# Kernel optimization log

Hardware: AMD Instinct MI355X
Metric: run time of the kernel (lower is better)

The kernel has to match this reference:

```python
import jax, jax.numpy as jnp
import numpy as np

B, T, V, D, H, L = 4, 2048, 99, 512, 8, 6
DH = D // H
OFFSET = 28  # size_puzzle_tokens = 1 + 26 + 1
GELU_C = 0.7978845608028654  # sqrt(2/pi)
EPS = 1e-5


def layernorm(x, w):
    m = jnp.mean(x, axis=-1, keepdims=True)
    v = jnp.mean(jnp.square(x - m), axis=-1, keepdims=True)
    return (x - m) / jnp.sqrt(v + EPS) * w


def new_gelu(x):
    return 0.5 * x * (1.0 + jnp.tanh(GELU_C * (x + 0.044715 * x ** 3)))


def setup_inputs() -> dict:
    key = jax.random.key(0)
    ks = jax.random.split(key, 12)
    s = 0.02
    return {
        'idx': jax.random.randint(ks[0], (B, T), 0, V),
        'targets': jax.random.randint(ks[1], (B, T), 0, V),
        'wte': jax.random.normal(ks[2], (V, D), jnp.float32) * s,   # tied with lm_head
        'wpe': jax.random.normal(ks[3], (T, D), jnp.float32) * s,
        'ln1_w': jnp.ones((L, D), jnp.float32),
        'attn_w': jax.random.normal(ks[4], (L, 3 * D, D), jnp.float32) * s,
        'proj_w': jax.random.normal(ks[5], (L, D, D), jnp.float32) * (s / np.sqrt(2 * L)),
        'ln2_w': jnp.ones((L, D), jnp.float32),
        'fc_w': jax.random.normal(ks[6], (L, 4 * D, D), jnp.float32) * s,
        'fc_proj_w': jax.random.normal(ks[7], (L, D, 4 * D), jnp.float32) * (s / np.sqrt(2 * L)),
        'lnf_w': jnp.ones((D,), jnp.float32),
    }


def _forward(idx, targets, wte, wpe, ln1_w, attn_w, proj_w, ln2_w, fc_w, fc_proj_w, lnf_w):
    t = idx.shape[1]
    x = wte[idx] + wpe[:t][None]  # [B,T,D]
    # mask: tril(ones(T+28, T)) narrowed from row 28 -> query i attends keys j <= i+28
    q_ids = jnp.arange(t)
    mask = (q_ids[None, :] <= q_ids[:, None] + OFFSET)  # [T,T]
    scale = 1.0 / np.sqrt(DH)

    def block(x, p):
        w1, wa, wp, w2, wf, wfp = p
        h = layernorm(x, w1)
        qkv = jnp.einsum('btc,oc->bto', h, wa)  # [B,T,3D]
        q, k, v = jnp.split(qkv, 3, axis=-1)
        q = q.reshape(B, t, H, DH)
        k = k.reshape(B, t, H, DH)
        v = v.reshape(B, t, H, DH)
        att = jnp.einsum('bqhd,bkhd->bhqk', q, k) * scale
        att = jnp.where(mask[None, None], att, -jnp.inf)
        att = jax.nn.softmax(att, axis=-1)
        y = jnp.einsum('bhqk,bkhd->bqhd', att, v).reshape(B, t, D)
        y = jnp.einsum('btc,oc->bto', y, wp)
        x = x + y
        h2 = layernorm(x, w2)
        m = new_gelu(jnp.einsum('btc,fc->btf', h2, wf))
        x = x + jnp.einsum('btf,cf->btc', m, wfp)
        return x, None

    x, _ = jax.lax.scan(block, x, (ln1_w, attn_w, proj_w, ln2_w, fc_w, fc_proj_w))
    x = layernorm(x, lnf_w)
    logits = jnp.einsum('btd,vd->btv', x, wte)

    # weighted cross entropy, ignore_index=-1
    ce_w = jnp.zeros((V,), jnp.float32).at[78:96].set(1.0).at[96].set(0.1)
    y = targets.reshape(-1)
    valid = (y != -1)
    yc = jnp.where(valid, y, 0)
    logp = jax.nn.log_softmax(logits.reshape(-1, V), axis=-1)
    nll = -jnp.take_along_axis(logp, yc[:, None], axis=1)[:, 0]
    wi = ce_w[yc] * valid.astype(jnp.float32)
    loss = jnp.sum(wi * nll) / jnp.sum(wi)
    return logits, loss


def reference(idx, targets, wte, wpe, ln1_w, attn_w, proj_w, ln2_w, fc_w, fc_proj_w, lnf_w):
    return _forward(idx, targets, wte, wpe, ln1_w, attn_w, proj_w, ln2_w, fc_w, fc_proj_w, lnf_w)
```

## Files before the change

kernel.cpp:

```cpp
#include <hip/hip_runtime.h>
#include <hip/hip_bf16.h>
#include <math.h>

#define BB 4
#define TT 2048
#define VV 99
#define DD 512
#define HH 8
#define LL 6
#define DHH 64
#define OFFS 28
#define ROWS (BB*TT)

typedef __hip_bfloat16 bf16;
typedef __attribute__((ext_vector_type(8))) short bf16x8;
typedef __attribute__((ext_vector_type(4))) short s16x4;
typedef __attribute__((ext_vector_type(4))) float f32x4;

__device__ __forceinline__ float b2f(bf16 x){ return __bfloat162float(x); }

__device__ __forceinline__ void async_copy16(const void* g, void* l){
    __builtin_amdgcn_global_load_lds(
        (const __attribute__((address_space(1))) unsigned int*)g,
        (__attribute__((address_space(3))) unsigned int*)l, 16, 0, 0);
}

__device__ __forceinline__ unsigned lds_off(const void* p){
    return (unsigned)(size_t)(const __attribute__((address_space(3))) char*)p;
}

#define TRD(dst, a, lit) asm volatile("ds_read_b64_tr_b16 %0, %1 offset:" lit \
                                      : "=v"(dst) : "v"(a) : "memory")
#define CAT8(lo, hi) ((bf16x8)__builtin_shufflevector((lo), (hi), 0,1,2,3,4,5,6,7))

__device__ __forceinline__ unsigned pk2(float a, float b){
    return ((unsigned)(unsigned short)__bfloat16_as_short(__float2bfloat16(a)))
         | ((unsigned)(unsigned short)__bfloat16_as_short(__float2bfloat16(b)) << 16);
}

__device__ __forceinline__ float wget(const void* w, int mode, size_t i){
    return mode ? b2f(((const bf16*)w)[i]) : ((const float*)w)[i];
}

__global__ void init_kernel(const unsigned int* __restrict__ ln1_bits, float* __restrict__ acc,
                            int* __restrict__ flag){
    acc[0] = 0.f; acc[1] = 0.f;
    flag[0] = (ln1_bits[0] == 0x3F800000u) ? 0 : 1;
}

__global__ __launch_bounds__(256) void wconv_kernel(const void* __restrict__ src,
                                                    bf16* __restrict__ dst, int n,
                                                    const int* __restrict__ flag){
    int mode = flag[0];
    size_t i0 = ((size_t)blockIdx.x*256 + threadIdx.x)*8;
    if (i0 >= (size_t)n) return;
    if (mode == 0){
        const float4* sp = (const float4*)((const float*)src + i0);
        float4 a = sp[0], b = sp[1];
        float f[8] = {a.x,a.y,a.z,a.w, b.x,b.y,b.z,b.w};
        union { short s[8]; uint4 u; } cv;
        #pragma unroll
        for (int k=0;k<8;++k) cv.s[k] = __bfloat16_as_short(__float2bfloat16(f[k]));
        *(uint4*)(dst + i0) = cv.u;
    } else {
        *(uint4*)(dst + i0) = *(const uint4*)((const bf16*)src + i0);
    }
}

__global__ void embed_kernel(const int* __restrict__ idx, const void* __restrict__ wte,
                             const void* __restrict__ wpe, float* __restrict__ x,
                             const int* __restrict__ flag){
    int mode = flag[0];
    int row = blockIdx.x;
    int t = row % TT;
    int tok = idx[row];
    int i = threadIdx.x;
    #pragma unroll
    for (int j = 0; j < 2; ++j){
        int d = i + j*256;
        x[(size_t)row*DD + d] = wget(wte, mode, (size_t)tok*DD + d)
                              + wget(wpe, mode, (size_t)t*DD + d);
    }
}

__global__ void ln_kernel(const float* __restrict__ x, const void* __restrict__ w,
                          size_t woff, bf16* __restrict__ out, const int* __restrict__ flag){
    int mode = flag[0];
    int row = blockIdx.x;
    int lane = threadIdx.x;
    const float* xr = x + (size_t)row*DD;
    float v[8];
    float s = 0.f;
    #pragma unroll
    for (int j=0;j<8;++j){ v[j] = xr[lane + j*64]; s += v[j]; }
    #pragma unroll
    for (int o=32;o;o>>=1) s += __shfl_xor(s,o);
    float mean = s * (1.0f/DD);
    float vs = 0.f;
    #pragma unroll
    for (int j=0;j<8;++j){ float d = v[j]-mean; vs += d*d; }
    #pragma unroll
    for (int o=32;o;o>>=1) vs += __shfl_xor(vs,o);
    float rstd = rsqrtf(vs*(1.0f/DD) + 1e-5f);
    #pragma unroll
    for (int j=0;j<8;++j){
        int d = lane + j*64;
        out[(size_t)row*DD + d] = __float2bfloat16((v[j]-mean)*rstd*wget(w,mode,woff+d));
    }
}

template<int EPI>
__global__ __launch_bounds__(256) void gemm_mfma(const bf16* __restrict__ A,
        const bf16* __restrict__ W, float* __restrict__ C, bf16* __restrict__ Cb,
        int M, int N, int K){
    __shared__ short As[128*32];
    __shared__ short Ws[128*32];
    int tid = threadIdx.x;
    int m0 = blockIdx.y * 128;
    int n0 = blockIdx.x * 128;
    int lane = tid & 63, wave = tid >> 6;
    int wm = (wave & 1) * 64, wn = (wave >> 1) * 64;
    int quad = lane >> 4, l16 = lane & 15;

    f32x4 acc[4][4] = {};

    int srow = wave*16 + (lane >> 2);
    int scol = (lane & 3) * 8;
    const bf16* ga = A + (size_t)(m0 + srow)*K + scol;
    const bf16* gw = W + (size_t)(n0 + srow)*K + scol;
    short* laA0 = &As[(wave*16)*32];
    short* laA1 = &As[(64 + wave*16)*32];
    short* laW0 = &Ws[(wave*16)*32];
    short* laW1 = &Ws[(64 + wave*16)*32];

    for (int k0 = 0; k0 < K; k0 += 32){
        __syncthreads();
        async_copy16(ga + k0,                 laA0);
        async_copy16(ga + (size_t)64*K + k0,  laA1);
        async_copy16(gw + k0,                 laW0);
        async_copy16(gw + (size_t)64*K + k0,  laW1);
        __syncthreads();

        bf16x8 af[4], bfr[4];
        #pragma unroll
        for (int mi=0;mi<4;++mi)
            af[mi] = *(const bf16x8*)&As[(wm + mi*16 + l16)*32 + quad*8];
        #pragma unroll
        for (int ni=0;ni<4;++ni)
            bfr[ni] = *(const bf16x8*)&Ws[(wn + ni*16 + l16)*32 + quad*8];
        #pragma unroll
        for (int mi=0;mi<4;++mi)
            #pragma unroll
            for (int ni=0;ni<4;++ni)
                acc[mi][ni] = __builtin_amdgcn_mfma_f32_16x16x32_bf16(af[mi], bfr[ni], acc[mi][ni], 0, 0, 0);
    }

    #pragma unroll
    for (int mi=0;mi<4;++mi){
        #pragma unroll
        for (int ni=0;ni<4;++ni){
            int mg = m0 + wm + mi*16 + quad*4;
            int ng = n0 + wn + ni*16 + l16;
            #pragma unroll
            for (int reg=0;reg<4;++reg){
                float val = acc[mi][ni][reg];
                size_t off = (size_t)(mg+reg)*N + ng;
                if (EPI==0){
                    Cb[off] = __float2bfloat16(val);
                } else {
                    float xx = val;
                    float u = 0.7978845608028654f*(xx + 0.044715f*xx*xx*xx);
                    Cb[off] = __float2bfloat16(0.5f*xx*(1.0f+tanhf(u)));
                }
            }
        }
    }
}

__global__ __launch_bounds__(256) void gemm_mfma64(const bf16* __restrict__ A,
        const bf16* __restrict__ W, float* __restrict__ C, int M, int N, int K){
    __shared__ short As[64*32];
    __shared__ short Ws[128*32];
    int tid = threadIdx.x;
    int m0 = blockIdx.y * 64;
    int n0 = blockIdx.x * 128;
    int lane = tid & 63, wave = tid >> 6;
    int wm = (wave & 1) * 32, wn = (wave >> 1) * 64;
    int quad = lane >> 4, l16 = lane & 15;

    f32x4 acc[2][4] = {};

    int srow = wave*16 + (lane >> 2);
    int scol = (lane & 3) * 8;
    const bf16* ga = A + (size_t)(m0 + srow)*K + scol;
    const bf16* gw = W + (size_t)(n0 + srow)*K + scol;
    short* laA0 = &As[(wave*16)*32];
    short* laW0 = &Ws[(wave*16)*32];
    short* laW1 = &Ws[(64 + wave*16)*32];

    for (int k0 = 0; k0 < K; k0 += 32){
        __syncthreads();
        async_copy16(ga + k0,                 laA0);
        async_copy16(gw + k0,                 laW0);
        async_copy16(gw + (size_t)64*K + k0,  laW1);
        __syncthreads();

        bf16x8 af[2], bfr[4];
        #pragma unroll
        for (int mi=0;mi<2;++mi)
            af[mi] = *(const bf16x8*)&As[(wm + mi*16 + l16)*32 + quad*8];
        #pragma unroll
        for (int ni=0;ni<4;++ni)
            bfr[ni] = *(const bf16x8*)&Ws[(wn + ni*16 + l16)*32 + quad*8];
        #pragma unroll
        for (int mi=0;mi<2;++mi)
            #pragma unroll
            for (int ni=0;ni<4;++ni)
                acc[mi][ni] = __builtin_amdgcn_mfma_f32_16x16x32_bf16(af[mi], bfr[ni], acc[mi][ni], 0, 0, 0);
    }

    #pragma unroll
    for (int mi=0;mi<2;++mi){
        #pragma unroll
        for (int ni=0;ni<4;++ni){
            int mg = m0 + wm + mi*16 + quad*4;
            int ng = n0 + wn + ni*16 + l16;
            #pragma unroll
            for (int reg=0;reg<4;++reg){
                C[(size_t)(mg+reg)*N + ng] += acc[mi][ni][reg];
            }
        }
    }
}

__global__ __launch_bounds__(256) void gemm_nt3(const bf16* __restrict__ A,
        const void* __restrict__ W, size_t woff, float* __restrict__ C,
        int M, int N, int K, const int* __restrict__ flag){
    int mode = flag[0];
    __shared__ float As[16][64];
    __shared__ float Wt[16][64];
    int m0 = blockIdx.y * 64;
    int n0 = blockIdx.x * 64;
    int t = threadIdx.x;
    int tx = t & 15, ty = t >> 4;
    float acc[4][4] = {};
    int am = t >> 2;
    int ak = (t & 3) * 4;

    for (int k0 = 0; k0 < K; k0 += 16){
        {
            const __hip_bfloat162* ap = (const __hip_bfloat162*)(A + (size_t)(m0+am)*K + k0 + ak);
            __hip_bfloat162 p0 = ap[0], p1 = ap[1];
            float2 f0 = __bfloat1622float2(p0), f1 = __bfloat1622float2(p1);
            As[ak+0][am]=f0.x; As[ak+1][am]=f0.y; As[ak+2][am]=f1.x; As[ak+3][am]=f1.y;
        }
        int wn = n0 + am;
        if (wn < N){
            size_t off = woff + (size_t)wn*K + k0 + ak;
            if (mode == 0){
                float4 wv = *(const float4*)((const float*)W + off);
                Wt[ak+0][am]=wv.x; Wt[ak+1][am]=wv.y; Wt[ak+2][am]=wv.z; Wt[ak+3][am]=wv.w;
            } else {
                const __hip_bfloat162* wp = (const __hip_bfloat162*)((const bf16*)W + off);
                __hip_bfloat162 p0 = wp[0], p1 = wp[1];
                float2 f0 = __bfloat1622float2(p0), f1 = __bfloat1622float2(p1);
                Wt[ak+0][am]=f0.x; Wt[ak+1][am]=f0.y; Wt[ak+2][am]=f1.x; Wt[ak+3][am]=f1.y;
            }
        } else {
            Wt[ak+0][am]=0.f; Wt[ak+1][am]=0.f; Wt[ak+2][am]=0.f; Wt[ak+3][am]=0.f;
        }
        __syncthreads();
        #pragma unroll
        for (int kk=0;kk<16;++kk){
            float a[4], b[4];
            #pragma unroll
            for (int i=0;i<4;++i) a[i]=As[kk][ty*4+i];
            #pragma unroll
            for (int j=0;j<4;++j) b[j]=Wt[kk][tx*4+j];
            #pragma unroll
            for (int i=0;i<4;++i)
                #pragma unroll
                for (int j=0;j<4;++j)
                    acc[i][j] += a[i]*b[j];
        }
        __syncthreads();
    }

    #pragma unroll
    for (int i=0;i<4;++i){
        int m = m0 + ty*4 + i;
        #pragma unroll
        for (int j=0;j<4;++j){
            int n = n0 + tx*4 + j;
            if (n >= N) continue;
            C[(size_t)m*N+n] = acc[i][j];
        }
    }
}

__global__ __launch_bounds__(256) void attn_mfma11(const bf16* __restrict__ qkv,
                                                   bf16* __restrict__ y){
    __shared__ __align__(16) short Ks[4][4096];
    __shared__ __align__(16) short Vs[4][4096];
    __shared__ __align__(16) short P2[4][1024];

    int tid = threadIdx.x;
    int lane = tid & 63, wave = tid >> 6;
    int quad = lane >> 4, l16 = lane & 15;

    int bi = blockIdx.x;
    int qt = 31 - (bi >> 5);
    int bh = bi & 31;
    int h = bh & 7;
    int b = bh >> 3;
    int q0 = qt * 64;
    size_t base = (size_t)b * TT * 1536;

    const bf16* qrow = qkv + base + (size_t)(q0 + wave*16 + l16)*1536 + h*64;
    bf16x8 aq0 = *(const bf16x8*)(qrow + quad*8);
    bf16x8 aq1 = *(const bf16x8*)(qrow + 32 + quad*8);

    int kj  = wave*16 + (lane>>3);
    int kgo = ((lane&7) ^ ((lane>>3)&7)) << 3;
    int vj  = ((lane>>3)&3)*8 + ((lane>>5)&1)*4 + ((lane>>1)&3);
    int vdo = wave*16 + ((lane&1)<<3);
    const bf16* ks0 = qkv + base + DD   + h*64 + (size_t)kj*1536 + kgo;
    const bf16* vs0 = qkv + base + 2*DD + h*64 + (size_t)vj*1536 + vdo;
    short* kd = &Ks[0][0] + wave*1024;
    short* vd = &Vs[0][0] + wave*1024;

#define STAGE(bb, j0s) { \
    const bf16* kk_ = ks0 + (size_t)(j0s)*1536; \
    const bf16* vv_ = vs0 + (size_t)(j0s)*1536; \
    short* kdd_ = kd + (bb)*4096; \
    short* vdd_ = vd + (bb)*4096; \
    async_copy16(kk_,                    kdd_); \
    async_copy16(kk_ + (size_t)8*1536,   kdd_ + 512); \
    async_copy16(vv_,                    vdd_); \
    async_copy16(vv_ + (size_t)32*1536,  vdd_ + 512); }

    f32x4 O[4] = {};
    float mr1 = -1e30f;
    float lr1 = 0.f;

    int jbmax = qt + 1; if (jbmax > 31) jbmax = 31;
    int NT = jbmax + 1;

    STAGE(0, 0);
    if (NT > 1) STAGE(1, 64);
    __syncthreads();

    unsigned l8 = (unsigned)(lane << 3);
    unsigned vbase = lds_off(&Vs[0][0]) + l8;
    char* pw = (char*)&P2[wave][0];
    int swz = (l16 & 7) << 4;
    int qg_row = q0 + wave*16 + l16;
    int sb = (quad<<4) | (quad<<2);

#define ATTN_BODY(tt) { \
    int t_ = (tt); \
    int j0 = t_ * 64; \
    const short* kb = &Ks[0][0] + (t_&3)*4096; \
    f32x4 s4[4]; \
    _Pragma("unroll") \
    for (int ni=0; ni<4; ++ni){ \
        int R = ni*16 + l16; \
        int ro = R*64; \
        int sw = R & 7; \
        bf16x8 bk0 = *(const bf16x8*)&kb[ro + ((quad       ^ sw)<<3)]; \
        bf16x8 bk1 = *(const bf16x8*)&kb[ro + (((quad + 4) ^ sw)<<3)]; \
        f32x4 z = {}; \
        z = __builtin_amdgcn_mfma_f32_16x16x32_bf16(bk0, aq0, z, 0, 0, 0); \
        z = __builtin_amdgcn_mfma_f32_16x16x32_bf16(bk1, aq1, z, 0, 0, 0); \
        s4[ni] = z; \
    } \
    float sc[4][4]; \
    bool bd = (j0 + 63 > q0 + OFFS); \
    _Pragma("unroll") \
    for (int ni=0; ni<4; ++ni){ \
        _Pragma("unroll") \
        for (int reg=0; reg<4; ++reg){ \
            float v = s4[ni][reg] * 0.125f; \
            if (bd){ \
                int jg = j0 + ni*16 + quad*4 + reg; \
                if (jg > qg_row + OFFS) v = -1e30f; \
            } \
            sc[ni][reg] = v; \
        } \
    } \
    float mn[4]; \
    _Pragma("unroll") \
    for (int ni=0; ni<4; ++ni) \
        mn[ni] = fmaxf(fmaxf(sc[ni][0], sc[ni][1]), fmaxf(sc[ni][2], sc[ni][3])); \
    float m16 = fmaxf(fmaxf(mn[0], mn[1]), fmaxf(mn[2], mn[3])); \
    m16 = fmaxf(m16, __shfl_xor(m16, 16)); \
    m16 = fmaxf(m16, __shfl_xor(m16, 32)); \
    float nm; \
    float alpha1 = 1.0f; \
    if (__all(m16 <= mr1 + 8.0f)){ \
        nm = mr1;             \
    } else { \
        nm = fmaxf(mr1, m16); \
        alpha1 = __expf(mr1 - nm); \
        mr1 = nm; \
        float al0 = __shfl(alpha1, sb); \
        float al1 = __shfl(alpha1, sb+1); \
        float al2 = __shfl(alpha1, sb+2); \
        float al3 = __shfl(alpha1, sb+3); \
        _Pragma("unroll") \
        for (int dt=0; dt<4; ++dt){ \
            O[dt][0] *= al0; O[dt][1] *= al1; O[dt][2] *= al2; O[dt][3] *= al3; \
        } \
    } \
    float rsn[4]; \
    _Pragma("unroll") \
    for (int ni=0; ni<4; ++ni){ \
        _Pragma("unroll") \
        for (int reg=0; reg<4; ++reg) \
            sc[ni][reg] = __expf(sc[ni][reg] - nm); \
        rsn[ni] = (sc[ni][0] + sc[ni][1]) + (sc[ni][2] + sc[ni][3]); \
    } \
    float rs1 = (rsn[0] + rsn[1]) + (rsn[2] + rsn[3]); \
    rs1 += __shfl_xor(rs1, 16); \
    rs1 += __shfl_xor(rs1, 32); \
    lr1 = lr1*alpha1 + rs1; \
    __builtin_amdgcn_sched_barrier(0); \
    unsigned va = vbase + (unsigned)((t_&3)*8192); \
    s16x4 t000,t001,t010,t011, t100,t101,t110,t111, \
          t200,t201,t210,t211, t300,t301,t310,t311; \
    TRD(t000, va, "0");    TRD(t001, va, "512");  TRD(t010, va, "1024"); TRD(t011, va, "1536"); \
    TRD(t100, va, "2048"); TRD(t101, va, "2560"); TRD(t110, va, "3072"); TRD(t111, va, "3584"); \
    TRD(t200, va, "4096"); TRD(t201, va, "4608"); TRD(t210, va, "5120"); TRD(t211, va, "5632"); \
    TRD(t300, va, "6144"); TRD(t301, va, "6656"); TRD(t310, va, "7168"); TRD(t311, va, "7680"); \
    _Pragma("unroll") \
    for (int ni=0; ni<4; ++ni){ \
        unsigned lo = pk2(sc[ni][0], sc[ni][1]); \
        unsigned hi = pk2(sc[ni][2], sc[ni][3]); \
        *(uint2*)(pw + (((l16<<7) + (ni<<5) + (quad<<3)) ^ swz)) = make_uint2(lo, hi); \
    } \
    bf16x8 ap0 = *(const bf16x8*)(pw + (((l16<<7)      + (quad<<4)) ^ swz)); \
    bf16x8 ap1 = *(const bf16x8*)(pw + (((l16<<7) + 64 + (quad<<4)) ^ swz)); \
    asm volatile("s_waitcnt lgkmcnt(0)" ::: "memory"); \
    __builtin_amdgcn_sched_barrier(0); \
    O[0] = __builtin_amdgcn_mfma_f32_16x16x32_bf16(ap0, CAT8(t000,t001), O[0], 0, 0, 0); \
    O[1] = __builtin_amdgcn_mfma_f32_16x16x32_bf16(ap0, CAT8(t100,t101), O[1], 0, 0, 0); \
    O[2] = __builtin_amdgcn_mfma_f32_16x16x32_bf16(ap0, CAT8(t200,t201), O[2], 0, 0, 0); \
    O[3] = __builtin_amdgcn_mfma_f32_16x16x32_bf16(ap0, CAT8(t300,t301), O[3], 0, 0, 0); \
    O[0] = __builtin_amdgcn_mfma_f32_16x16x32_bf16(ap1, CAT8(t010,t011), O[0], 0, 0, 0); \
    O[1] = __builtin_amdgcn_mfma_f32_16x16x32_bf16(ap1, CAT8(t110,t111), O[1], 0, 0, 0); \
    O[2] = __builtin_amdgcn_mfma_f32_16x16x32_bf16(ap1, CAT8(t210,t211), O[2], 0, 0, 0); \
    O[3] = __builtin_amdgcn_mfma_f32_16x16x32_bf16(ap1, CAT8(t310,t311), O[3], 0, 0, 0); }

    for (int tp = 0; tp < NT; tp += 2){
        if (tp+2 < NT) STAGE((tp+2)&3, (tp+2)*64);
        if (tp+3 < NT) STAGE((tp+3)&3, (tp+3)*64);
        ATTN_BODY(tp);
        if (tp+1 < NT) ATTN_BODY(tp+1);
        __syncthreads();
    }
#undef ATTN_BODY
#undef STAGE

    float invl = 1.0f / lr1;
    float in0 = __shfl(invl, sb);
    float in1 = __shfl(invl, sb+1);
    float in2 = __shfl(invl, sb+2);
    float in3 = __shfl(invl, sb+3);
    float inv[4] = {in0, in1, in2, in3};
    #pragma unroll
    for (int dt=0; dt<4; ++dt){
        #pragma unroll
        for (int reg=0; reg<4; ++reg){
            int qg = q0 + wave*16 + quad*4 + reg;
            y[((size_t)b*TT + qg)*DD + h*64 + dt*16 + l16] =
                __float2bfloat16(O[dt][reg] * inv[reg]);
        }
    }
}

__global__ void loss_kernel(const float* __restrict__ logits, const int* __restrict__ targets,
                            float* __restrict__ acc){
    int row = blockIdx.x;
    int lane = threadIdx.x;
    int yt = targets[row];
    const float* lp = logits + (size_t)row*VV;
    float e0 = (lane < VV)    ? lp[lane]    : -1e30f;
    float e1 = (lane+64 < VV) ? lp[lane+64] : -1e30f;
    float mx = fmaxf(e0,e1);
    #pragma unroll
    for (int o=32;o;o>>=1) mx = fmaxf(mx, __shfl_xor(mx,o));
    float se = 0.f;
    if (lane < VV)    se += __expf(e0-mx);
    if (lane+64 < VV) se += __expf(e1-mx);
    #pragma unroll
    for (int o=32;o;o>>=1) se += __shfl_xor(se,o);
    if (lane == 0 && yt >= 0){
        float wi = (yt>=78 && yt<96) ? 1.0f : (yt==96 ? 0.1f : 0.0f);
        if (wi > 0.f){
            float ly = lp[yt];
            float nll = -(ly - mx - logf(se));
            atomicAdd(&acc[0], wi*nll);
            atomicAdd(&acc[1], wi);
        }
    }
}

__global__ void fin_loss(const float* __restrict__ acc, float* __restrict__ out){
    out[0] = acc[0]/acc[1];
}

extern "C" void kernel_launch(void* const* d_in, const int* in_sizes, int n_in,
                              void* d_out, int out_size, void* d_ws, size_t ws_size,
                              hipStream_t stream){
    const int*  idx     = (const int*) d_in[0];
    const int*  targets = (const int*) d_in[1];
    const void* wte     = d_in[2];
    const void* wpe     = d_in[3];
    const void* ln1_w   = d_in[4];
    const void* attn_w  = d_in[5];
    const void* proj_w  = d_in[6];
    const void* ln2_w   = d_in[7];
    const void* fc_w    = d_in[8];
    const void* fcp_w   = d_in[9];
    const void* lnf_w   = d_in[10];
    float* out = (float*)d_out;

    float* ws   = (float*)d_ws;
    float* ACC  = ws;
    int*   FLAG = (int*)(ws + 4);
    bf16*  Hb   = (bf16*)(ws + 16);
    float* X    = ws + 2097168;
    bf16*  BIG  = (bf16*)(ws + 6291472);
    bf16*  WB   = (bf16*)(ws + 14680080);

    const int ATT_S = 3*DD*DD;
    const int PRJ_S = DD*DD;
    const int FC_S  = 4*DD*DD;
    bf16* WB_att = WB;
    bf16* WB_prj = WB + (size_t)6*ATT_S;
    bf16* WB_fc  = WB_prj + (size_t)6*PRJ_S;
    bf16* WB_fcp = WB_fc  + (size_t)6*FC_S;

    init_kernel<<<1,1,0,stream>>>((const unsigned int*)ln1_w, ACC, FLAG);
    wconv_kernel<<<(6*ATT_S)/2048,256,0,stream>>>(attn_w, WB_att, 6*ATT_S, FLAG);
    wconv_kernel<<<(6*PRJ_S)/2048,256,0,stream>>>(proj_w, WB_prj, 6*PRJ_S, FLAG);
    wconv_kernel<<<(6*FC_S)/2048,256,0,stream>>>(fc_w,  WB_fc,  6*FC_S, FLAG);
    wconv_kernel<<<(6*FC_S)/2048,256,0,stream>>>(fcp_w, WB_fcp, 6*FC_S, FLAG);
    embed_kernel<<<ROWS,256,0,stream>>>(idx, wte, wpe, X, FLAG);
    for (int l=0; l<LL; ++l){
        ln_kernel<<<ROWS,64,0,stream>>>(X, ln1_w, (size_t)l*DD, Hb, FLAG);
        gemm_mfma<0><<<dim3(3*DD/128, ROWS/128),256,0,stream>>>(Hb, WB_att + (size_t)l*ATT_S,
                                                                nullptr, BIG, ROWS, 3*DD, DD);
        attn_mfma11<<<dim3(BB*HH*32),256,0,stream>>>(BIG, Hb);
        gemm_mfma64<<<dim3(DD/128, ROWS/64),256,0,stream>>>(Hb, WB_prj + (size_t)l*PRJ_S,
                                                            X, ROWS, DD, DD);
        ln_kernel<<<ROWS,64,0,stream>>>(X, ln2_w, (size_t)l*DD, Hb, FLAG);
        gemm_mfma<2><<<dim3(4*DD/128, ROWS/128),256,0,stream>>>(Hb, WB_fc + (size_t)l*FC_S,
                                                                nullptr, BIG, ROWS, 4*DD, DD);
        gemm_mfma64<<<dim3(DD/128, ROWS/64),256,0,stream>>>(BIG, WB_fcp + (size_t)l*FC_S,
                                                            X, ROWS, DD, 4*DD);
    }
    ln_kernel<<<ROWS,64,0,stream>>>(X, lnf_w, 0, Hb, FLAG);
    gemm_nt3<<<dim3((VV+63)/64, ROWS/64),256,0,stream>>>(Hb, wte, 0, out, ROWS, VV, DD, FLAG);
    loss_kernel<<<ROWS,64,0,stream>>>(out, targets, ACC);
    fin_loss<<<1,1,0,stream>>>(ACC, out + (size_t)ROWS*VV);
}
```

Baseline: 1.503 ms.

## Double-buffer LDS in MFMA GEMMs and move logits GEMM onto MFMA

Both MFMA GEMM kernels now use two LDS buffers, so the async global-to-LDS copy for the next K-slice is issued before the current slice's MFMAs, and only one barrier runs per iteration instead of two. The scalar fp32 logits GEMM is replaced by an MFMA kernel that reads a bf16 copy of wte, zero-padded to 128 rows by a new conversion kernel. This targets exposed load latency and the slow scalar logits path, at the cost of twice the LDS per block (possibly lowering occupancy), an extra workspace region and bf16 rounding of the tied embedding weights.

```diff
diff --git a/kernel.cpp b/kernel.cpp
--- a/kernel.cpp
+++ b/kernel.cpp
@@ -67,6 +67,22 @@
     }
 }
 
+__global__ __launch_bounds__(256) void wconv_pad(const void* __restrict__ src,
+                                                 bf16* __restrict__ dst, int n, int npad,
+                                                 const int* __restrict__ flag){
+    int mode = flag[0];
+    size_t i0 = ((size_t)blockIdx.x*256 + threadIdx.x)*8;
+    if (i0 >= (size_t)npad) return;
+    union { short s[8]; uint4 u; } cv;
+    #pragma unroll
+    for (int k=0;k<8;++k){
+        size_t i = i0 + k;
+        float f = (i < (size_t)n) ? wget(src, mode, i) : 0.f;
+        cv.s[k] = __bfloat16_as_short(__float2bfloat16(f));
+    }
+    *(uint4*)(dst + i0) = cv.u;
+}
+
 __global__ void embed_kernel(const int* __restrict__ idx, const void* __restrict__ wte,
                              const void* __restrict__ wpe, float* __restrict__ x,
                              const int* __restrict__ flag){
@@ -113,8 +129,8 @@
 __global__ __launch_bounds__(256) void gemm_mfma(const bf16* __restrict__ A,
         const bf16* __restrict__ W, float* __restrict__ C, bf16* __restrict__ Cb,
         int M, int N, int K){
-    __shared__ short As[128*32];
-    __shared__ short Ws[128*32];
+    __shared__ short As[2][128*32];
+    __shared__ short Ws[2][128*32];
     int tid = threadIdx.x;
     int m0 = blockIdx.y * 128;
     int n0 = blockIdx.x * 128;
@@ -128,32 +144,36 @@
     int scol = (lane & 3) * 8;
     const bf16* ga = A + (size_t)(m0 + srow)*K + scol;
     const bf16* gw = W + (size_t)(n0 + srow)*K + scol;
-    short* laA0 = &As[(wave*16)*32];
-    short* laA1 = &As[(64 + wave*16)*32];
-    short* laW0 = &Ws[(wave*16)*32];
-    short* laW1 = &Ws[(64 + wave*16)*32];
+
+#define GSTAGE(bb, kk) { \
+    async_copy16(ga + (kk),                 &As[bb][(wave*16)*32]); \
+    async_copy16(ga + (size_t)64*K + (kk),  &As[bb][(64 + wave*16)*32]); \
+    async_copy16(gw + (kk),                 &Ws[bb][(wave*16)*32]); \
+    async_copy16(gw + (size_t)64*K + (kk),  &Ws[bb][(64 + wave*16)*32]); }
+
+    GSTAGE(0, 0);
+    __syncthreads();
+    int cur = 0;
 
     for (int k0 = 0; k0 < K; k0 += 32){
-        __syncthreads();
-        async_copy16(ga + k0,                 laA0);
-        async_copy16(ga + (size_t)64*K + k0,  laA1);
-        async_copy16(gw + k0,                 laW0);
-        async_copy16(gw + (size_t)64*K + k0,  laW1);
-        __syncthreads();
+        if (k0 + 32 < K) GSTAGE(cur^1, k0 + 32);
 
         bf16x8 af[4], bfr[4];
         #pragma unroll
         for (int mi=0;mi<4;++mi)
-            af[mi] = *(const bf16x8*)&As[(wm + mi*16 + l16)*32 + quad*8];
+            af[mi] = *(const bf16x8*)&As[cur][(wm + mi*16 + l16)*32 + quad*8];
         #pragma unroll
         for (int ni=0;ni<4;++ni)
-            bfr[ni] = *(const bf16x8*)&Ws[(wn + ni*16 + l16)*32 + quad*8];
+            bfr[ni] = *(const bf16x8*)&Ws[cur][(wn + ni*16 + l16)*32 + quad*8];
         #pragma unroll
         for (int mi=0;mi<4;++mi)
             #pragma unroll
             for (int ni=0;ni<4;++ni)
                 acc[mi][ni] = __builtin_amdgcn_mfma_f32_16x16x32_bf16(af[mi], bfr[ni], acc[mi][ni], 0, 0, 0);
-    }
+
+        if (k0 + 32 < K){ __syncthreads(); cur ^= 1; }
+    }
+#undef GSTAGE
 
     #pragma unroll
     for (int mi=0;mi<4;++mi){
@@ -179,8 +199,8 @@
 
 __global__ __launch_bounds__(256) void gemm_mfma64(const bf16* __restrict__ A,
         const bf16* __restrict__ W, float* __restrict__ C, int M, int N, int K){
-    __shared__ short As[64*32];
-    __shared__ short Ws[128*32];
+    __shared__ short As[2][64*32];
+    __shared__ short Ws[2][128*32];
     int tid = threadIdx.x;
     int m0 = blockIdx.y * 64;
     int n0 = blockIdx.x * 128;
@@ -194,30 +214,35 @@
     int scol = (lane & 3) * 8;
     const bf16* ga = A + (size_t)(m0 + srow)*K + scol;
     const bf16* gw = W + (size_t)(n0 + srow)*K + scol;
-    short* laA0 = &As[(wave*16)*32];
-    short* laW0 = &Ws[(wave*16)*32];
-    short* laW1 = &Ws[(64 + wave*16)*32];
+
+#define GSTAGE64(bb, kk) { \
+    async_copy16(ga + (kk),                 &As[bb][(wave*16)*32]); \
+    async_copy16(gw + (kk),                 &Ws[bb][(wave*16)*32]); \
+    async_copy16(gw + (size_t)64*K + (kk),  &Ws[bb][(64 + wave*16)*32]); }
+
+    GSTAGE64(0, 0);
+    __syncthreads();
+    int cur = 0;
 
     for (int k0 = 0; k0 < K; k0 += 32){
-        __syncthreads();
-        async_copy16(ga + k0,                 laA0);
-        async_copy16(gw + k0,                 laW0);
-        async_copy16(gw + (size_t)64*K + k0,  laW1);
-        __syncthreads();
+        if (k0 + 32 < K) GSTAGE64(cur^1, k0 + 32);
 
         bf16x8 af[2], bfr[4];
         #pragma unroll
         for (int mi=0;mi<2;++mi)
-            af[mi] = *(const bf16x8*)&As[(wm + mi*16 + l16)*32 + quad*8];
+            af[mi] = *(const bf16x8*)&As[cur][(wm + mi*16 + l16)*32 + quad*8];
         #pragma unroll
         for (int ni=0;ni<4;++ni)
-            bfr[ni] = *(const bf16x8*)&Ws[(wn + ni*16 + l16)*32 + quad*8];
+            bfr[ni] = *(const bf16x8*)&Ws[cur][(wn + ni*16 + l16)*32 + quad*8];
         #pragma unroll
         for (int mi=0;mi<2;++mi)
             #pragma unroll
             for (int ni=0;ni<4;++ni)
                 acc[mi][ni] = __builtin_amdgcn_mfma_f32_16x16x32_bf16(af[mi], bfr[ni], acc[mi][ni], 0, 0, 0);
-    }
+
+        if (k0 + 32 < K){ __syncthreads(); cur ^= 1; }
+    }
+#undef GSTAGE64
 
     #pragma unroll
     for (int mi=0;mi<2;++mi){
@@ -233,67 +258,64 @@
     }
 }
 
-__global__ __launch_bounds__(256) void gemm_nt3(const bf16* __restrict__ A,
-        const void* __restrict__ W, size_t woff, float* __restrict__ C,
-        int M, int N, int K, const int* __restrict__ flag){
-    int mode = flag[0];
-    __shared__ float As[16][64];
-    __shared__ float Wt[16][64];
-    int m0 = blockIdx.y * 64;
-    int n0 = blockIdx.x * 64;
-    int t = threadIdx.x;
-    int tx = t & 15, ty = t >> 4;
-    float acc[4][4] = {};
-    int am = t >> 2;
-    int ak = (t & 3) * 4;
-
-    for (int k0 = 0; k0 < K; k0 += 16){
-        {
-            const __hip_bfloat162* ap = (const __hip_bfloat162*)(A + (size_t)(m0+am)*K + k0 + ak);
-            __hip_bfloat162 p0 = ap[0], p1 = ap[1];
-            float2 f0 = __bfloat1622float2(p0), f1 = __bfloat1622float2(p1);
-            As[ak+0][am]=f0.x; As[ak+1][am]=f0.y; As[ak+2][am]=f1.x; As[ak+3][am]=f1.y;
-        }
-        int wn = n0 + am;
-        if (wn < N){
-            size_t off = woff + (size_t)wn*K + k0 + ak;
-            if (mode == 0){
-                float4 wv = *(const float4*)((const float*)W + off);
-                Wt[ak+0][am]=wv.x; Wt[ak+1][am]=wv.y; Wt[ak+2][am]=wv.z; Wt[ak+3][am]=wv.w;
-            } else {
-                const __hip_bfloat162* wp = (const __hip_bfloat162*)((const bf16*)W + off);
-                __hip_bfloat162 p0 = wp[0], p1 = wp[1];
-                float2 f0 = __bfloat1622float2(p0), f1 = __bfloat1622float2(p1);
-                Wt[ak+0][am]=f0.x; Wt[ak+1][am]=f0.y; Wt[ak+2][am]=f1.x; Wt[ak+3][am]=f1.y;
-            }
-        } else {
-            Wt[ak+0][am]=0.f; Wt[ak+1][am]=0.f; Wt[ak+2][am]=0.f; Wt[ak+3][am]=0.f;
-        }
-        __syncthreads();
-        #pragma unroll
-        for (int kk=0;kk<16;++kk){
-            float a[4], b[4];
+__global__ __launch_bounds__(256) void gemm_logits(const bf16* __restrict__ A,
+        const bf16* __restrict__ W, float* __restrict__ C){
+    const int K = DD;
+    __shared__ short As[2][128*32];
+    __shared__ short Ws[2][128*32];
+    int tid = threadIdx.x;
+    int m0 = blockIdx.y * 128;
+    int lane = tid & 63, wave = tid >> 6;
+    int wm = (wave & 1) * 64, wn = (wave >> 1) * 64;
+    int quad = lane >> 4, l16 = lane & 15;
+
+    f32x4 acc[4][4] = {};
+
+    int srow = wave*16 + (lane >> 2);
+    int scol = (lane & 3) * 8;
+    const bf16* ga = A + (size_t)(m0 + srow)*K + scol;
+    const bf16* gw = W + (size_t)srow*K + scol;
+
+#define GSTAGEL(bb, kk) { \
+    async_copy16(ga + (kk),                 &As[bb][(wave*16)*32]); \
+    async_copy16(ga + (size_t)64*K + (kk),  &As[bb][(64 + wave*16)*32]); \
+    async_copy16(gw + (kk),                 &Ws[bb][(wave*16)*32]); \
+    async_copy16(gw + (size_t)64*K + (kk),  &Ws[bb][(64 + wave*16)*32]); }
+
+    GSTAGEL(0, 0);
+    __syncthreads();
+    int cur = 0;
+
+    for (int k0 = 0; k0 < K; k0 += 32){
+        if (k0 + 32 < K) GSTAGEL(cur^1, k0 + 32);
+
+        bf16x8 af[4], bfr[4];
+        #pragma unroll
+        for (int mi=0;mi<4;++mi)
+            af[mi] = *(const bf16x8*)&As[cur][(wm + mi*16 + l16)*32 + quad*8];
+        #pragma unroll
+        for (int ni=0;ni<4;++ni)
+            bfr[ni] = *(const bf16x8*)&Ws[cur][(wn + ni*16 + l16)*32 + quad*8];
+        #pragma unroll
+        for (int mi=0;mi<4;++mi)
             #pragma unroll
-            for (int i=0;i<4;++i) a[i]=As[kk][ty*4+i];
+            for (int ni=0;ni<4;++ni)
+                acc[mi][ni] = __builtin_amdgcn_mfma_f32_16x16x32_bf16(af[mi], bfr[ni], acc[mi][ni], 0, 0, 0);
+
+        if (k0 + 32 < K){ __syncthreads(); cur ^= 1; }
+    }
+#undef GSTAGEL
+
+    #pragma unroll
+    for (int mi=0;mi<4;++mi){
+        #pragma unroll
+        for (int ni=0;ni<4;++ni){
+            int mg = m0 + wm + mi*16 + quad*4;
+            int ng = wn + ni*16 + l16;
+            if (ng >= VV) continue;
             #pragma unroll
-            for (int j=0;j<4;++j) b[j]=Wt[kk][tx*4+j];
-            #pragma unroll
-            for (int i=0;i<4;++i)
-                #pragma unroll
-                for (int j=0;j<4;++j)
-                    acc[i][j] += a[i]*b[j];
-        }
-        __syncthreads();
-    }
-
-    #pragma unroll
-    for (int i=0;i<4;++i){
-        int m = m0 + ty*4 + i;
-        #pragma unroll
-        for (int j=0;j<4;++j){
-            int n = n0 + tx*4 + j;
-            if (n >= N) continue;
-            C[(size_t)m*N+n] = acc[i][j];
+            for (int reg=0;reg<4;++reg)
+                C[(size_t)(mg+reg)*VV + ng] = acc[mi][ni][reg];
         }
     }
 }
@@ -540,12 +562,14 @@
     bf16* WB_prj = WB + (size_t)6*ATT_S;
     bf16* WB_fc  = WB_prj + (size_t)6*PRJ_S;
     bf16* WB_fcp = WB_fc  + (size_t)6*FC_S;
+    bf16* WB_wte = WB_fcp + (size_t)6*FC_S;
 
     init_kernel<<<1,1,0,stream>>>((const unsigned int*)ln1_w, ACC, FLAG);
     wconv_kernel<<<(6*ATT_S)/2048,256,0,stream>>>(attn_w, WB_att, 6*ATT_S, FLAG);
     wconv_kernel<<<(6*PRJ_S)/2048,256,0,stream>>>(proj_w, WB_prj, 6*PRJ_S, FLAG);
     wconv_kernel<<<(6*FC_S)/2048,256,0,stream>>>(fc_w,  WB_fc,  6*FC_S, FLAG);
     wconv_kernel<<<(6*FC_S)/2048,256,0,stream>>>(fcp_w, WB_fcp, 6*FC_S, FLAG);
+    wconv_pad<<<(128*DD)/2048,256,0,stream>>>(wte, WB_wte, VV*DD, 128*DD, FLAG);
     embed_kernel<<<ROWS,256,0,stream>>>(idx, wte, wpe, X, FLAG);
     for (int l=0; l<LL; ++l){
         ln_kernel<<<ROWS,64,0,stream>>>(X, ln1_w, (size_t)l*DD, Hb, FLAG);
@@ -561,7 +585,7 @@
                                                             X, ROWS, DD, 4*DD);
     }
     ln_kernel<<<ROWS,64,0,stream>>>(X, lnf_w, 0, Hb, FLAG);
-    gemm_nt3<<<dim3((VV+63)/64, ROWS/64),256,0,stream>>>(Hb, wte, 0, out, ROWS, VV, DD, FLAG);
+    gemm_logits<<<dim3(1, ROWS/128),256,0,stream>>>(Hb, WB_wte, out);
     loss_kernel<<<ROWS,64,0,stream>>>(out, targets, ACC);
     fin_loss<<<1,1,0,stream>>>(ACC, out + (size_t)ROWS*VV);
 }
```

New measurement: 1.650 ms. +9.8%, slower.
